# Performance work log

Measured on AMD Instinct MI355X. Metric: run time of the kernel, lower is better.

Reference implementation:

```python
import jax, jax.numpy as jnp
import numpy as np

TOPK = (1, 5)


def setup_inputs() -> dict:
    key = jax.random.key(0)
    kZ, kY, kI = jax.random.split(key, 3)
    b, s, f = 9600, 2400, 4096
    Z = jax.random.normal(kZ, (b, f), dtype=jnp.float32)
    Y = jax.random.normal(kY, (s, f), dtype=jnp.float32)
    y_idxs = jax.random.randint(kI, (b,), 0, s, dtype=jnp.int64 if jax.config.jax_enable_x64 else jnp.int32)
    test_y_idxs = jnp.arange(s, dtype=y_idxs.dtype)
    return {"Z": Z, "y_idxs": y_idxs, "Y": Y, "test_y_idxs": test_y_idxs}


def reference(Z, y_idxs, Y, test_y_idxs):
    # L2-normalize rows, then cosine similarity as a single GEMM instead of the
    # original broadcasted (b, s, f) F.cosine_similarity intermediate.
    eps = 1e-8
    Zn = Z / jnp.maximum(jnp.linalg.norm(Z, axis=-1, keepdims=True), eps)
    Yn = Y / jnp.maximum(jnp.linalg.norm(Y, axis=-1, keepdims=True), eps)
    similarity = Zn @ Yn.T  # (b, s)

    # labels[i] = position of y_idxs[i] inside test_y_idxs (each appears exactly once)
    labels = jnp.argmax(y_idxs[None, :] == test_y_idxs[:, None], axis=0)  # (b,)

    accs = []
    for k in TOPK:
        _, topk_idx = jax.lax.top_k(similarity, k)  # (b, k)
        hit = jnp.any(topk_idx == labels[:, None], axis=1)
        accs.append(jnp.mean(hit.astype(jnp.float32)))
    return jnp.stack(accs)
```

## Files before the change

kernel.cpp:

```cpp
#include <hip/hip_runtime.h>

#define INT_MAX_C 0x7fffffff

typedef __attribute__((ext_vector_type(8))) short s16x8;
typedef __attribute__((ext_vector_type(4))) float f32x4;

__global__ void k_init_inv(int* inv, int s) {
  int j = blockIdx.x * 256 + threadIdx.x;
  if (j < s) inv[j] = INT_MAX_C;
}

__global__ void k_scatter(const int* __restrict__ tyi, int* __restrict__ inv, int s) {
  int j = blockIdx.x * 256 + threadIdx.x;
  if (j < s) {
    int v = tyi[j];
    if (v >= 0 && v < s) atomicMin(&inv[v], j);
  }
}

__global__ void k_labels(const int* __restrict__ yi, const int* __restrict__ inv,
                         int* __restrict__ labels, int b, int s) {
  int i = blockIdx.x * 256 + threadIdx.x;
  if (i < b) {
    int v = yi[i];
    int lab = 0;
    if (v >= 0 && v < s) { int p = inv[v]; if (p != INT_MAX_C) lab = p; }
    labels[i] = lab;
  }
}

__global__ __launch_bounds__(256) void k_ynorm(const float* __restrict__ Y,
                                               float* __restrict__ invY, int f) {
  int j = blockIdx.x;
  const float* row = Y + (size_t)j * f;
  float ss = 0.f;
  for (int k = threadIdx.x * 4; k < f; k += 256 * 4) {
    float4 v = *(const float4*)(row + k);
    ss += v.x * v.x + v.y * v.y + v.z * v.z + v.w * v.w;
  }
  int lane = threadIdx.x & 63, wid = threadIdx.x >> 6;
#pragma unroll
  for (int o = 32; o > 0; o >>= 1) ss += __shfl_down(ss, o, 64);
  __shared__ float sh[4];
  if (lane == 0) sh[wid] = ss;
  __syncthreads();
  if (threadIdx.x == 0) {
    float tot = sh[0] + sh[1] + sh[2] + sh[3];
    invY[j] = 1.f / fmaxf(sqrtf(tot), 1e-8f);
  }
}

__global__ __launch_bounds__(256) void k_zrow(
    const float* __restrict__ Z, const float* __restrict__ Y,
    const int* __restrict__ labels, const float* __restrict__ invY,
    float* __restrict__ invZ, float* __restrict__ simL, int f) {
  int i = blockIdx.x;
  int lab = labels[i];
  const float* zr = Z + (size_t)i * f;
  const float* yr = Y + (size_t)lab * f;
  float ss = 0.f, dt = 0.f;
  for (int k = threadIdx.x * 4; k < f; k += 256 * 4) {
    float4 z = *(const float4*)(zr + k);
    float4 y = *(const float4*)(yr + k);
    ss += z.x * z.x + z.y * z.y + z.z * z.z + z.w * z.w;
    dt += z.x * y.x + z.y * y.y + z.z * y.z + z.w * y.w;
  }
  int lane = threadIdx.x & 63, wid = threadIdx.x >> 6;
#pragma unroll
  for (int o = 32; o > 0; o >>= 1) {
    ss += __shfl_down(ss, o, 64);
    dt += __shfl_down(dt, o, 64);
  }
  __shared__ float shs[4], shd[4];
  if (lane == 0) { shs[wid] = ss; shd[wid] = dt; }
  __syncthreads();
  if (threadIdx.x == 0) {
    float S = shs[0] + shs[1] + shs[2] + shs[3];
    float D = shd[0] + shd[1] + shd[2] + shd[3];
    float iz = 1.f / fmaxf(sqrtf(S), 1e-8f);
    invZ[i] = iz;
    simL[i] = D * iz * invY[lab];
  }
}

__device__ __forceinline__ uint rne_hi_bits(uint u) {
  return (u + 0x7fffu + ((u >> 16) & 1u)) & 0xffff0000u;
}

__device__ __forceinline__ void split_pack8(float4 a, float4 b, uint4& hi, uint4& lo) {
  float v[8] = {a.x, a.y, a.z, a.w, b.x, b.y, b.z, b.w};
  uint h[8], l[8];
#pragma unroll
  for (int i = 0; i < 8; ++i) {
    uint u = __float_as_uint(v[i]);
    uint rh = rne_hi_bits(u);
    h[i] = rh;
    float d = v[i] - __uint_as_float(rh);
    uint ud = __float_as_uint(d);
    l[i] = (ud + 0x7fffu + ((ud >> 16) & 1u));
  }
  hi = make_uint4((h[0] >> 16) | h[1], (h[2] >> 16) | h[3],
                  (h[4] >> 16) | h[5], (h[6] >> 16) | h[7]);
  lo = make_uint4((l[0] >> 16) | (l[1] & 0xffff0000u),
                  (l[2] >> 16) | (l[3] & 0xffff0000u),
                  (l[4] >> 16) | (l[5] & 0xffff0000u),
                  (l[6] >> 16) | (l[7] & 0xffff0000u));
}

__global__ __launch_bounds__(256) void k_packZ(const float* __restrict__ Z,
                                               char* __restrict__ Zpan,
                                               int f, int nkc) {
  int r = blockIdx.x * 4 + (threadIdx.x >> 6);
  int lane = threadIdx.x & 63;
  int rt = r >> 7, rl = r & 127;
  char* pan = Zpan + (size_t)rt * nkc * 16384;
  const float* row = Z + (size_t)r * f;
  int niter = f >> 9;
  for (int j = 0; j < niter; ++j) {
    int gq = lane + 64 * j;
    float4 v0 = *(const float4*)(row + gq * 8);
    float4 v1 = *(const float4*)(row + gq * 8 + 4);
    uint4 h, l;
    split_pack8(v0, v1, h, l);
    int kc = gq >> 2, kq = gq & 3;
    size_t off = (size_t)kc * 16384 + rl * 64 + ((kq ^ ((rl >> 1) & 3)) << 4);
    *(uint4*)(pan + off) = h;
    *(uint4*)(pan + off + 8192) = l;
  }
}

__global__ __launch_bounds__(256) void k_packY(const float* __restrict__ Y,
                                               char* __restrict__ Ypan,
                                               float* __restrict__ invY,
                                               int s, int f, int nkc) {
  int r = blockIdx.x * 4 + (threadIdx.x >> 6);
  int lane = threadIdx.x & 63;
  int ct = r >> 8, rl = r & 255;
  char* pan = Ypan + (size_t)ct * nkc * 32768;
  const float* row = Y + (size_t)r * f;
  const bool ok = r < s;
  float ss = 0.f;
  int niter = f >> 9;
  for (int j = 0; j < niter; ++j) {
    int gq = lane + 64 * j;
    float4 v0 = {}, v1 = {};
    if (ok) {
      v0 = *(const float4*)(row + gq * 8);
      v1 = *(const float4*)(row + gq * 8 + 4);
    }
    ss += v0.x * v0.x + v0.y * v0.y + v0.z * v0.z + v0.w * v0.w +
          v1.x * v1.x + v1.y * v1.y + v1.z * v1.z + v1.w * v1.w;
    uint4 h, l;
    split_pack8(v0, v1, h, l);
    int kc = gq >> 2, kq = gq & 3;
    size_t off = (size_t)kc * 32768 + rl * 64 + ((kq ^ ((rl >> 1) & 3)) << 4);
    *(uint4*)(pan + off) = h;
    *(uint4*)(pan + off + 16384) = l;
  }
  if (ok) {
#pragma unroll
    for (int o = 32; o > 0; o >>= 1) ss += __shfl_down(ss, o, 64);
    if (lane == 0) invY[r] = 1.f / fmaxf(sqrtf(ss), 1e-8f);
  }
}

__device__ __forceinline__ void dma16(const void* g, void* l) {
  __builtin_amdgcn_global_load_lds((const __attribute__((address_space(1))) unsigned int*)g,
                                   (__attribute__((address_space(3))) unsigned int*)l,
                                   16, 0, 0);
}

__global__ __launch_bounds__(256, 2) void k_gemm_rank_pan(
    const char* __restrict__ Zpan, const char* __restrict__ Ypan,
    const float* __restrict__ invZ, const float* __restrict__ invY,
    const float* __restrict__ simL, const int* __restrict__ labels,
    int* __restrict__ rank, int b, int s, int nkc) {
  __shared__ ushort SMu[24576];
  char* SMb = (char*)SMu;
  __shared__ float sL[128], sIz[128];
  __shared__ int sLab[128], sCnt[128];

  const int t = threadIdx.x;
  const int row0 = blockIdx.x * 128;
  const int col0 = blockIdx.y * 256;

  if (t < 128) {
    int gi = row0 + t;
    sL[t] = simL[gi]; sIz[t] = invZ[gi]; sLab[t] = labels[gi];
    sCnt[t] = 0;
  }

  const char* srcA = Zpan + (size_t)blockIdx.x * nkc * 16384 + t * 16;
  const char* srcB = Ypan + (size_t)blockIdx.y * nkc * 32768 + t * 16;

  const int lane = t & 63;
  const int wv = t >> 6;
  const int wr = wv >> 1, wc = wv & 1;
  const int fm = lane & 15, quad = lane >> 4;

  int aoff[4], boff[8];
#pragma unroll
  for (int i = 0; i < 4; ++i) {
    int r = wr * 64 + i * 16 + fm;
    aoff[i] = r * 64 + ((quad ^ ((r >> 1) & 3)) << 4);
  }
#pragma unroll
  for (int i = 0; i < 8; ++i) {
    int c = wc * 128 + i * 16 + fm;
    boff[i] = 16384 + c * 64 + ((quad ^ ((c >> 1) & 3)) << 4);
  }

  f32x4 acc[4][8] = {};

  for (int kt = 0; kt < nkc; ++kt) {
    __syncthreads();
#pragma unroll
    for (int j = 0; j < 4; ++j) dma16(srcA + j * 4096, SMb + j * 4096 + t * 16);
#pragma unroll
    for (int j = 0; j < 8; ++j) dma16(srcB + j * 4096, SMb + 16384 + j * 4096 + t * 16);
    srcA += 16384; srcB += 32768;
    __syncthreads();

    s16x8 ah[4], al[4];
#pragma unroll
    for (int i = 0; i < 4; ++i) {
      ah[i] = *(const s16x8*)(SMb + aoff[i]);
      al[i] = *(const s16x8*)(SMb + aoff[i] + 8192);
    }
#pragma unroll
    for (int cc = 0; cc < 8; ++cc) {
      s16x8 bh = *(const s16x8*)(SMb + boff[cc]);
      s16x8 bl = *(const s16x8*)(SMb + boff[cc] + 16384);
#pragma unroll
      for (int rr = 0; rr < 4; ++rr) {
        acc[rr][cc] = __builtin_amdgcn_mfma_f32_16x16x32_bf16(ah[rr], bh, acc[rr][cc], 0, 0, 0);
        acc[rr][cc] = __builtin_amdgcn_mfma_f32_16x16x32_bf16(ah[rr], bl, acc[rr][cc], 0, 0, 0);
        acc[rr][cc] = __builtin_amdgcn_mfma_f32_16x16x32_bf16(al[rr], bh, acc[rr][cc], 0, 0, 0);
      }
    }
  }

  float iYc[8]; int gjc[8];
#pragma unroll
  for (int c = 0; c < 8; ++c) {
    int gj = col0 + wc * 128 + c * 16 + fm;
    gjc[c] = gj;
    iYc[c] = (gj < s) ? invY[gj] : 0.f;
  }

#pragma unroll
  for (int rr = 0; rr < 4; ++rr) {
#pragma unroll
    for (int reg = 0; reg < 4; ++reg) {
      int li = wr * 64 + rr * 16 + quad * 4 + reg;
      float iz = sIz[li], sl = sL[li];
      int lab = sLab[li];
      int cnt = 0;
#pragma unroll
      for (int c = 0; c < 8; ++c) {
        int gj = gjc[c];
        if (gj < s && gj != lab) {
          float sim = acc[rr][c][reg] * iz * iYc[c];
          cnt += (sim > sl || (sim == sl && gj < lab)) ? 1 : 0;
        }
      }
      cnt += __shfl_down(cnt, 8, 16);
      cnt += __shfl_down(cnt, 4, 16);
      cnt += __shfl_down(cnt, 2, 16);
      cnt += __shfl_down(cnt, 1, 16);
      if (fm == 0 && cnt) atomicAdd(&sCnt[li], cnt);
    }
  }
  __syncthreads();
  if (t < 128) {
    int gi = row0 + t;
    if (sCnt[t]) atomicAdd(&rank[gi], sCnt[t]);
  }
}

#define TMF 128
#define TNF 128
#define BKF 32
#define SKF 40

__global__ __launch_bounds__(256) void k_gemm_rank_v2(
    const float* __restrict__ Z, const float* __restrict__ Y,
    const float* __restrict__ invZ, const float* __restrict__ invY,
    const float* __restrict__ simL, const int* __restrict__ labels,
    int* __restrict__ rank, int b, int s, int f) {
  __shared__ short Ah[TMF * SKF], Al[TMF * SKF], Bh[TNF * SKF], Bl[TNF * SKF];
  __shared__ float sL[TMF], sIz[TMF];
  __shared__ int sLab[TMF], sCnt[TMF];

  const int t = threadIdx.x;
  const int row0 = blockIdx.y * TMF;
  const int col0 = blockIdx.x * TNF;

  if (t < TMF) {
    int gi = row0 + t;
    if (gi < b) { sL[t] = simL[gi]; sIz[t] = invZ[gi]; sLab[t] = labels[gi]; }
    else        { sL[t] = 0.f;      sIz[t] = 0.f;      sLab[t] = -1; }
    sCnt[t] = 0;
  }

  const int srow  = t >> 1;
  const int skoff = (t & 1) << 4;
  const bool zok = (row0 + srow) < b;
  const bool yok = (col0 + srow) < s;
  const float* zp = Z + (size_t)(row0 + srow) * f + skoff;
  const float* yp = Y + (size_t)(col0 + srow) * f + skoff;

  const int lane = t & 63;
  const int wv = t >> 6;
  const int wr = wv >> 1, wc = wv & 1;
  const int fm = lane & 15, quad = lane >> 4;

  f32x4 acc[4][4] = {};

  for (int kt = 0; kt < f; kt += BKF) {
    float4 z0 = {}, z1 = {}, z2 = {}, z3 = {};
    float4 y0 = {}, y1 = {}, y2 = {}, y3 = {};
    if (zok) {
      z0 = *(const float4*)(zp + 0); z1 = *(const float4*)(zp + 4);
      z2 = *(const float4*)(zp + 8); z3 = *(const float4*)(zp + 12);
    }
    if (yok) {
      y0 = *(const float4*)(yp + 0); y1 = *(const float4*)(yp + 4);
      y2 = *(const float4*)(yp + 8); y3 = *(const float4*)(yp + 12);
    }
    zp += BKF; yp += BKF;

    __syncthreads();

    uint4 h, l;
    split_pack8(z0, z1, h, l);
    *(uint4*)(Ah + srow * SKF + skoff)     = h;
    *(uint4*)(Al + srow * SKF + skoff)     = l;
    split_pack8(z2, z3, h, l);
    *(uint4*)(Ah + srow * SKF + skoff + 8) = h;
    *(uint4*)(Al + srow * SKF + skoff + 8) = l;
    split_pack8(y0, y1, h, l);
    *(uint4*)(Bh + srow * SKF + skoff)     = h;
    *(uint4*)(Bl + srow * SKF + skoff)     = l;
    split_pack8(y2, y3, h, l);
    *(uint4*)(Bh + srow * SKF + skoff + 8) = h;
    *(uint4*)(Bl + srow * SKF + skoff + 8) = l;

    __syncthreads();

    s16x8 ah[4], al4[4], bh[4], bl4[4];
#pragma unroll
    for (int rr = 0; rr < 4; ++rr) {
      int ar = wr * 64 + rr * 16 + fm;
      ah[rr]  = *(const s16x8*)(Ah + ar * SKF + quad * 8);
      al4[rr] = *(const s16x8*)(Al + ar * SKF + quad * 8);
    }
#pragma unroll
    for (int cc = 0; cc < 4; ++cc) {
      int br = wc * 64 + cc * 16 + fm;
      bh[cc]  = *(const s16x8*)(Bh + br * SKF + quad * 8);
      bl4[cc] = *(const s16x8*)(Bl + br * SKF + quad * 8);
    }
#pragma unroll
    for (int rr = 0; rr < 4; ++rr)
#pragma unroll
      for (int cc = 0; cc < 4; ++cc) {
        acc[rr][cc] = __builtin_amdgcn_mfma_f32_16x16x32_bf16(ah[rr],  bh[cc],  acc[rr][cc], 0, 0, 0);
        acc[rr][cc] = __builtin_amdgcn_mfma_f32_16x16x32_bf16(ah[rr],  bl4[cc], acc[rr][cc], 0, 0, 0);
        acc[rr][cc] = __builtin_amdgcn_mfma_f32_16x16x32_bf16(al4[rr], bh[cc],  acc[rr][cc], 0, 0, 0);
      }
  }

  float iYc[4]; int gjc[4];
#pragma unroll
  for (int c = 0; c < 4; ++c) {
    int gj = col0 + wc * 64 + c * 16 + fm;
    gjc[c] = gj;
    iYc[c] = (gj < s) ? invY[gj] : 0.f;
  }

#pragma unroll
  for (int rr = 0; rr < 4; ++rr) {
#pragma unroll
    for (int reg = 0; reg < 4; ++reg) {
      int li = wr * 64 + rr * 16 + quad * 4 + reg;
      int gi = row0 + li;
      int cnt = 0;
      if (gi < b) {
        float iz = sIz[li], sl = sL[li];
        int lab = sLab[li];
#pragma unroll
        for (int c = 0; c < 4; ++c) {
          int gj = gjc[c];
          if (gj < s && gj != lab) {
            float sim = acc[rr][c][reg] * iz * iYc[c];
            cnt += (sim > sl || (sim == sl && gj < lab)) ? 1 : 0;
          }
        }
      }
      cnt += __shfl_down(cnt, 8, 16);
      cnt += __shfl_down(cnt, 4, 16);
      cnt += __shfl_down(cnt, 2, 16);
      cnt += __shfl_down(cnt, 1, 16);
      if (fm == 0 && cnt) atomicAdd(&sCnt[li], cnt);
    }
  }
  __syncthreads();
  if (t < TMF) {
    int gi = row0 + t;
    if (gi < b && sCnt[t]) atomicAdd(&rank[gi], sCnt[t]);
  }
}

__global__ __launch_bounds__(256) void k_final(const int* __restrict__ rank,
                                               float* __restrict__ out, int b) {
  int c1 = 0, c5 = 0;
  for (int i = threadIdx.x; i < b; i += 256) {
    int r = rank[i];
    c1 += (r < 1);
    c5 += (r < 5);
  }
  int lane = threadIdx.x & 63, wid = threadIdx.x >> 6;
#pragma unroll
  for (int o = 32; o > 0; o >>= 1) {
    c1 += __shfl_down(c1, o, 64);
    c5 += __shfl_down(c5, o, 64);
  }
  __shared__ int s1[4], s5[4];
  if (lane == 0) { s1[wid] = c1; s5[wid] = c5; }
  __syncthreads();
  if (threadIdx.x == 0) {
    int t1 = s1[0] + s1[1] + s1[2] + s1[3];
    int t5 = s5[0] + s5[1] + s5[2] + s5[3];
    out[0] = (float)t1 / (float)b;
    out[1] = (float)t5 / (float)b;
  }
}

extern "C" void kernel_launch(void* const* d_in, const int* in_sizes, int n_in,
                              void* d_out, int out_size, void* d_ws, size_t ws_size,
                              hipStream_t stream) {
  const float* Z  = (const float*)d_in[0];
  const int* yi   = (const int*)d_in[1];
  const float* Y  = (const float*)d_in[2];
  const int* tyi  = (const int*)d_in[3];
  const int b = in_sizes[1];
  const int s = in_sizes[3];
  const int f = in_sizes[0] / b;
  float* out = (float*)d_out;

  char* p = (char*)d_ws;
  size_t used = 0;
  auto alloc = [&](size_t bytes) {
    char* r = p;
    size_t a = (bytes + 255) & ~(size_t)255;
    p += a; used += a;
    return r;
  };
  int* inv     = (int*)alloc((size_t)s * 4);
  int* labels  = (int*)alloc((size_t)b * 4);
  int* rank    = (int*)alloc((size_t)b * 4);
  float* invY  = (float*)alloc((size_t)s * 4);
  float* invZ  = (float*)alloc((size_t)b * 4);
  float* simL  = (float*)alloc((size_t)b * 4);

  const int nkc = f >> 5;
  const int nrt = b / 128;
  const int nct = (s + 255) / 256;
  const int rows_pad = nct * 256;
  const size_t zpan_sz = (size_t)nrt * nkc * 16384;
  const size_t ypan_sz = (size_t)nct * nkc * 32768;
  const size_t need = used + zpan_sz + ypan_sz + 1024;
  const bool use_pan = (ws_size >= need) && (b % 128 == 0) && (f % 512 == 0) &&
                       (s % 4 == 0);

  hipMemsetAsync(rank, 0, (size_t)b * 4, stream);
  k_init_inv<<<(s + 255) / 256, 256, 0, stream>>>(inv, s);
  k_scatter<<<(s + 255) / 256, 256, 0, stream>>>(tyi, inv, s);
  k_labels<<<(b + 255) / 256, 256, 0, stream>>>(yi, inv, labels, b, s);

  if (use_pan) {
    char* Zpan = (char*)alloc(zpan_sz);
    char* Ypan = (char*)alloc(ypan_sz);
    k_packY<<<rows_pad / 4, 256, 0, stream>>>(Y, Ypan, invY, s, f, nkc);
    k_packZ<<<b / 4, 256, 0, stream>>>(Z, Zpan, f, nkc);
    k_zrow<<<b, 256, 0, stream>>>(Z, Y, labels, invY, invZ, simL, f);
    dim3 grid(nrt, nct);
    k_gemm_rank_pan<<<grid, 256, 0, stream>>>(Zpan, Ypan, invZ, invY, simL,
                                              labels, rank, b, s, nkc);
  } else {
    k_ynorm<<<s, 256, 0, stream>>>(Y, invY, f);
    k_zrow<<<b, 256, 0, stream>>>(Z, Y, labels, invY, invZ, simL, f);
    dim3 grid((s + TNF - 1) / TNF, (b + TMF - 1) / TMF);
    k_gemm_rank_v2<<<grid, 256, 0, stream>>>(Z, Y, invZ, invY, simL, labels,
                                             rank, b, s, f);
  }
  k_final<<<1, 256, 0, stream>>>(rank, out, b);
}
```

Before: 915.0 us.

## Shrink GEMM column tile to 192 for 3 blocks/CU and fuse zrow into packZ

Changes the GEMM column tile from 256 to 192 columns, so the panel layout, LDS footprint and accumulator count shrink and launch bounds allow 3 blocks per CU. With s=2400 this gives 13 column tiles with less padding waste and more resident blocks. Separately, the Z norm and label-similarity computation (k_zrow) is folded into k_packZ, so Z is read once instead of twice. The cost is lower per-block data reuse and an extra labeled-Y row read inside the pack kernel.

```diff
diff --git a/kernel.cpp b/kernel.cpp
--- a/kernel.cpp
+++ b/kernel.cpp
@@ -108,18 +108,32 @@
 }
 
 __global__ __launch_bounds__(256) void k_packZ(const float* __restrict__ Z,
+                                               const float* __restrict__ Y,
+                                               const int* __restrict__ labels,
+                                               const float* __restrict__ invY,
                                                char* __restrict__ Zpan,
+                                               float* __restrict__ invZ,
+                                               float* __restrict__ simL,
                                                int f, int nkc) {
   int r = blockIdx.x * 4 + (threadIdx.x >> 6);
   int lane = threadIdx.x & 63;
   int rt = r >> 7, rl = r & 127;
   char* pan = Zpan + (size_t)rt * nkc * 16384;
   const float* row = Z + (size_t)r * f;
+  int lab = labels[r];
+  const float* yrow = Y + (size_t)lab * f;
+  float ss = 0.f, dt = 0.f;
   int niter = f >> 9;
   for (int j = 0; j < niter; ++j) {
     int gq = lane + 64 * j;
     float4 v0 = *(const float4*)(row + gq * 8);
     float4 v1 = *(const float4*)(row + gq * 8 + 4);
+    float4 y0 = *(const float4*)(yrow + gq * 8);
+    float4 y1 = *(const float4*)(yrow + gq * 8 + 4);
+    ss += v0.x * v0.x + v0.y * v0.y + v0.z * v0.z + v0.w * v0.w +
+          v1.x * v1.x + v1.y * v1.y + v1.z * v1.z + v1.w * v1.w;
+    dt += v0.x * y0.x + v0.y * y0.y + v0.z * y0.z + v0.w * y0.w +
+          v1.x * y1.x + v1.y * y1.y + v1.z * y1.z + v1.w * y1.w;
     uint4 h, l;
     split_pack8(v0, v1, h, l);
     int kc = gq >> 2, kq = gq & 3;
@@ -127,6 +141,16 @@
     *(uint4*)(pan + off) = h;
     *(uint4*)(pan + off + 8192) = l;
   }
+#pragma unroll
+  for (int o = 32; o > 0; o >>= 1) {
+    ss += __shfl_down(ss, o, 64);
+    dt += __shfl_down(dt, o, 64);
+  }
+  if (lane == 0) {
+    float iz = 1.f / fmaxf(sqrtf(ss), 1e-8f);
+    invZ[r] = iz;
+    simL[r] = dt * iz * invY[lab];
+  }
 }
 
 __global__ __launch_bounds__(256) void k_packY(const float* __restrict__ Y,
@@ -135,8 +159,8 @@
                                                int s, int f, int nkc) {
   int r = blockIdx.x * 4 + (threadIdx.x >> 6);
   int lane = threadIdx.x & 63;
-  int ct = r >> 8, rl = r & 255;
-  char* pan = Ypan + (size_t)ct * nkc * 32768;
+  int ct = r / 192, rl = r % 192;
+  char* pan = Ypan + (size_t)ct * nkc * 24576;
   const float* row = Y + (size_t)r * f;
   const bool ok = r < s;
   float ss = 0.f;
@@ -153,9 +177,9 @@
     uint4 h, l;
     split_pack8(v0, v1, h, l);
     int kc = gq >> 2, kq = gq & 3;
-    size_t off = (size_t)kc * 32768 + rl * 64 + ((kq ^ ((rl >> 1) & 3)) << 4);
+    size_t off = (size_t)kc * 24576 + rl * 64 + ((kq ^ ((rl >> 1) & 3)) << 4);
     *(uint4*)(pan + off) = h;
-    *(uint4*)(pan + off + 16384) = l;
+    *(uint4*)(pan + off + 12288) = l;
   }
   if (ok) {
 #pragma unroll
@@ -170,19 +194,19 @@
                                    16, 0, 0);
 }
 
-__global__ __launch_bounds__(256, 2) void k_gemm_rank_pan(
+__global__ __launch_bounds__(256, 3) void k_gemm_rank_pan(
     const char* __restrict__ Zpan, const char* __restrict__ Ypan,
     const float* __restrict__ invZ, const float* __restrict__ invY,
     const float* __restrict__ simL, const int* __restrict__ labels,
     int* __restrict__ rank, int b, int s, int nkc) {
-  __shared__ ushort SMu[24576];
+  __shared__ ushort SMu[20480];
   char* SMb = (char*)SMu;
   __shared__ float sL[128], sIz[128];
   __shared__ int sLab[128], sCnt[128];
 
   const int t = threadIdx.x;
   const int row0 = blockIdx.x * 128;
-  const int col0 = blockIdx.y * 256;
+  const int col0 = blockIdx.y * 192;
 
   if (t < 128) {
     int gi = row0 + t;
@@ -191,34 +215,34 @@
   }
 
   const char* srcA = Zpan + (size_t)blockIdx.x * nkc * 16384 + t * 16;
-  const char* srcB = Ypan + (size_t)blockIdx.y * nkc * 32768 + t * 16;
+  const char* srcB = Ypan + (size_t)blockIdx.y * nkc * 24576 + t * 16;
 
   const int lane = t & 63;
   const int wv = t >> 6;
   const int wr = wv >> 1, wc = wv & 1;
   const int fm = lane & 15, quad = lane >> 4;
 
-  int aoff[4], boff[8];
+  int aoff[4], boff[6];
 #pragma unroll
   for (int i = 0; i < 4; ++i) {
     int r = wr * 64 + i * 16 + fm;
     aoff[i] = r * 64 + ((quad ^ ((r >> 1) & 3)) << 4);
   }
 #pragma unroll
-  for (int i = 0; i < 8; ++i) {
-    int c = wc * 128 + i * 16 + fm;
+  for (int i = 0; i < 6; ++i) {
+    int c = wc * 96 + i * 16 + fm;
     boff[i] = 16384 + c * 64 + ((quad ^ ((c >> 1) & 3)) << 4);
   }
 
-  f32x4 acc[4][8] = {};
+  f32x4 acc[4][6] = {};
 
   for (int kt = 0; kt < nkc; ++kt) {
     __syncthreads();
 #pragma unroll
     for (int j = 0; j < 4; ++j) dma16(srcA + j * 4096, SMb + j * 4096 + t * 16);
 #pragma unroll
-    for (int j = 0; j < 8; ++j) dma16(srcB + j * 4096, SMb + 16384 + j * 4096 + t * 16);
-    srcA += 16384; srcB += 32768;
+    for (int j = 0; j < 6; ++j) dma16(srcB + j * 4096, SMb + 16384 + j * 4096 + t * 16);
+    srcA += 16384; srcB += 24576;
     __syncthreads();
 
     s16x8 ah[4], al[4];
@@ -228,9 +252,9 @@
       al[i] = *(const s16x8*)(SMb + aoff[i] + 8192);
     }
 #pragma unroll
-    for (int cc = 0; cc < 8; ++cc) {
+    for (int cc = 0; cc < 6; ++cc) {
       s16x8 bh = *(const s16x8*)(SMb + boff[cc]);
-      s16x8 bl = *(const s16x8*)(SMb + boff[cc] + 16384);
+      s16x8 bl = *(const s16x8*)(SMb + boff[cc] + 12288);
 #pragma unroll
       for (int rr = 0; rr < 4; ++rr) {
         acc[rr][cc] = __builtin_amdgcn_mfma_f32_16x16x32_bf16(ah[rr], bh, acc[rr][cc], 0, 0, 0);
@@ -240,11 +264,10 @@
     }
   }
 
-  float iYc[8]; int gjc[8];
-#pragma unroll
-  for (int c = 0; c < 8; ++c) {
-    int gj = col0 + wc * 128 + c * 16 + fm;
-    gjc[c] = gj;
+  float iYc[6];
+#pragma unroll
+  for (int c = 0; c < 6; ++c) {
+    int gj = col0 + wc * 96 + c * 16 + fm;
     iYc[c] = (gj < s) ? invY[gj] : 0.f;
   }
 
@@ -257,8 +280,8 @@
       int lab = sLab[li];
       int cnt = 0;
 #pragma unroll
-      for (int c = 0; c < 8; ++c) {
-        int gj = gjc[c];
+      for (int c = 0; c < 6; ++c) {
+        int gj = col0 + wc * 96 + c * 16 + fm;
         if (gj < s && gj != lab) {
           float sim = acc[rr][c][reg] * iz * iYc[c];
           cnt += (sim > sl || (sim == sl && gj < lab)) ? 1 : 0;
@@ -466,10 +489,10 @@
 
   const int nkc = f >> 5;
   const int nrt = b / 128;
-  const int nct = (s + 255) / 256;
-  const int rows_pad = nct * 256;
+  const int nct = (s + 191) / 192;
+  const int rows_pad = nct * 192;
   const size_t zpan_sz = (size_t)nrt * nkc * 16384;
-  const size_t ypan_sz = (size_t)nct * nkc * 32768;
+  const size_t ypan_sz = (size_t)nct * nkc * 24576;
   const size_t need = used + zpan_sz + ypan_sz + 1024;
   const bool use_pan = (ws_size >= need) && (b % 128 == 0) && (f % 512 == 0) &&
                        (s % 4 == 0);
@@ -483,8 +506,7 @@
     char* Zpan = (char*)alloc(zpan_sz);
     char* Ypan = (char*)alloc(ypan_sz);
     k_packY<<<rows_pad / 4, 256, 0, stream>>>(Y, Ypan, invY, s, f, nkc);
-    k_packZ<<<b / 4, 256, 0, stream>>>(Z, Zpan, f, nkc);
-    k_zrow<<<b, 256, 0, stream>>>(Z, Y, labels, invY, invZ, simL, f);
+    k_packZ<<<b / 4, 256, 0, stream>>>(Z, Y, labels, invY, Zpan, invZ, simL, f, nkc);
     dim3 grid(nrt, nct);
     k_gemm_rank_pan<<<grid, 256, 0, stream>>>(Zpan, Ypan, invZ, invY, simL,
                                               labels, rank, b, s, nkc);
```

Measured after the change: 839.2 us. 8.3% less time.
